# Optimization experiments

Hardware: AMD Instinct MI355X
Metric: run time of the kernel (lower is better)

Reference implementation:

```python
import jax, jax.numpy as jnp
import numpy as np

S = 64          # per-axis section size; sections = [64, 64, 64, 64], D = 256
N_TOK = 131072  # tokens
D = 256
FREQS = np.power(10000.0, -np.arange(18, dtype=np.float64) / 18.0).astype(np.float32)


def setup_inputs() -> dict:
    key = jax.random.key(0)
    k1, k2, k3 = jax.random.split(key, 3)
    return {
        "keyEmbeddings": jax.random.normal(k1, (N_TOK, D), dtype=jnp.float32),
        "queryEmbeddings": jax.random.normal(k2, (N_TOK, D), dtype=jnp.float32),
        "locations": jax.random.normal(k3, (N_TOK, 7), dtype=jnp.float32),
        "freqs": jnp.asarray(FREQS),
    }


def _rot(A, B, ang):
    # performRotation: newA = cos*A + sin*B ; newB = cos*B - sin*A
    c, s = jnp.cos(ang), jnp.sin(ang)
    return c * A + s * B, c * B - s * A


def reference(keyEmbeddings, queryEmbeddings, locations, freqs):
    K, Q, loc = keyEmbeddings, queryEmbeddings, locations
    a4, a5, a6 = loc[:, 4:5], loc[:, 5:6], loc[:, 6:7]

    # ---- stage 1: 3D axis-pair rotations ----
    qx, qy, qz, qr = Q[:, :S], Q[:, S:2*S], Q[:, 2*S:3*S], Q[:, 3*S:]
    qx, qy = _rot(qx, qy, -a4)
    qx, qz = _rot(qx, qz, -a5)
    qy, qz = _rot(qy, qz, -a6)
    Q = jnp.concatenate([qx, qy, qz, qr], axis=-1)

    kx, ky, kz, kr = K[:, :S], K[:, S:2*S], K[:, 2*S:3*S], K[:, 3*S:]
    ky, kz = _rot(ky, kz, a6)
    kx, kz = _rot(kx, kz, a5)
    kx, ky = _rot(kx, ky, a4)
    K = jnp.concatenate([kx, ky, kz, kr], axis=-1)

    # ---- stage 2: multi-frequency per-channel-pair rotations ----
    F = freqs.shape[0]
    P = 7 * F  # number of channel pairs (2*P <= D)
    ang = (loc[:, :, None] * freqs[None, None, :]).reshape(loc.shape[0], P)  # [N, P]
    c, s = jnp.cos(ang), jnp.sin(ang)

    # Faithful to the original in-place update: second element of each pair
    # uses the already-updated first element.
    Ka, Kb = K[:, 0:2*P:2], K[:, 1:2*P:2]
    Ka2 = c * Ka + s * Kb
    Kb2 = c * Kb - s * Ka2
    Kp = jnp.stack([Ka2, Kb2], axis=-1).reshape(K.shape[0], 2 * P)
    K = jnp.concatenate([Kp, K[:, 2*P:]], axis=-1)

    Qa, Qb = Q[:, 0:2*P:2], Q[:, 1:2*P:2]
    Qa2 = c * Qa - s * Qb
    Qb2 = c * Qb + s * Qa2
    Qp = jnp.stack([Qa2, Qb2], axis=-1).reshape(Q.shape[0], 2 * P)
    Q = jnp.concatenate([Qp, Q[:, 2*P:]], axis=-1)

    return K, Q
```

## Files before the change

### kernel.cpp

```cpp
#include <hip/hip_runtime.h>
#include <math.h>


namespace {

constexpr int kNTok = 131072;
constexpr int kD = 256;

__device__ __forceinline__ void pair_rot(int p, const float* lrow,
                                         const float* __restrict__ freqs,
                                         float& ka, float& kb,
                                         float& qa, float& qb) {
    const int j = p / 18;
    const int f = p - j * 18;
    const float ang = lrow[j] * freqs[f];
    float s, c;
    __sincosf(ang, &s, &c);
    float ka2 = fmaf(s, kb, c * ka);
    kb = fmaf(-s, ka2, c * kb);
    ka = ka2;
    float qa2 = fmaf(-s, qb, c * qa);
    qb = fmaf(s, qa2, c * qb);
    qa = qa2;
}

}

__global__ __launch_bounds__(256) void rope_kernel(
    const float* __restrict__ Kin, const float* __restrict__ Qin,
    const float* __restrict__ loc, const float* __restrict__ freqs,
    float* __restrict__ Kout, float* __restrict__ Qout)
{
    const int gtid = blockIdx.x * blockDim.x + threadIdx.x;
    const int n = gtid >> 4;
    const int u = gtid & 15;
    if (n >= kNTok) return;

    const size_t row = (size_t)n * kD;
    const float4* K4 = (const float4*)(Kin + row);
    const float4* Q4 = (const float4*)(Qin + row);
    float4 kx = K4[u], ky = K4[16 + u], kz = K4[32 + u], kr = K4[48 + u];
    float4 qx = Q4[u], qy = Q4[16 + u], qz = Q4[32 + u], qr = Q4[48 + u];

    const float* lrow = loc + (size_t)n * 7;
    float s4, c4, s5, c5, s6, c6;
    __sincosf(lrow[4], &s4, &c4);
    __sincosf(lrow[5], &s5, &c5);
    __sincosf(lrow[6], &s6, &c6);

#define ROT3(i)                                      \
    {                                                \
        float x = kx.i, y = ky.i, z = kz.i;          \
        float y1 = fmaf(s6, z, c6 * y);              \
        float z1 = fmaf(-s6, y, c6 * z);             \
        float x1 = fmaf(s5, z1, c5 * x);             \
        float z2 = fmaf(-s5, x, c5 * z1);            \
        kx.i = fmaf(s4, y1, c4 * x1);                \
        ky.i = fmaf(-s4, x1, c4 * y1);               \
        kz.i = z2;                                   \
        x = qx.i; y = qy.i; z = qz.i;                \
        float xq1 = fmaf(-s4, y, c4 * x);            \
        float yq1 = fmaf(s4, x, c4 * y);             \
        float xq2 = fmaf(-s5, z, c5 * xq1);          \
        float zq1 = fmaf(s5, xq1, c5 * z);           \
        qx.i = xq2;                                  \
        qy.i = fmaf(-s6, zq1, c6 * yq1);             \
        qz.i = fmaf(s6, yq1, c6 * zq1);              \
    }
    ROT3(x) ROT3(y) ROT3(z) ROT3(w)
#undef ROT3

    const int p0 = 2 * u;
    pair_rot(p0,          lrow, freqs, kx.x, kx.y, qx.x, qx.y);
    pair_rot(p0 + 1,      lrow, freqs, kx.z, kx.w, qx.z, qx.w);
    pair_rot(32 + p0,     lrow, freqs, ky.x, ky.y, qy.x, qy.y);
    pair_rot(32 + p0 + 1, lrow, freqs, ky.z, ky.w, qy.z, qy.w);
    pair_rot(64 + p0,     lrow, freqs, kz.x, kz.y, qz.x, qz.y);
    pair_rot(64 + p0 + 1, lrow, freqs, kz.z, kz.w, qz.z, qz.w);
    if (u < 15) {
        pair_rot(96 + p0,     lrow, freqs, kr.x, kr.y, qr.x, qr.y);
        pair_rot(96 + p0 + 1, lrow, freqs, kr.z, kr.w, qr.z, qr.w);
    }

    float4* Ko = (float4*)(Kout + row);
    float4* Qo = (float4*)(Qout + row);
    Ko[u] = kx; Ko[16 + u] = ky; Ko[32 + u] = kz; Ko[48 + u] = kr;
    Qo[u] = qx; Qo[16 + u] = qy; Qo[32 + u] = qz; Qo[48 + u] = qr;
}

extern "C" void kernel_launch(void* const* d_in, const int* in_sizes, int n_in,
                              void* d_out, int out_size, void* d_ws, size_t ws_size,
                              hipStream_t stream) {
    const float* K     = (const float*)d_in[0];
    const float* Q     = (const float*)d_in[1];
    const float* loc   = (const float*)d_in[2];
    const float* freqs = (const float*)d_in[3];
    float* Kout = (float*)d_out;
    float* Qout = Kout + (size_t)kNTok * kD;

    const int threads = 256;
    const int total_threads = kNTok * 16;
    const int blocks = (total_threads + threads - 1) / threads;
    hipLaunchKernelGGL(rope_kernel, dim3(blocks), dim3(threads), 0, stream,
                       K, Q, loc, freqs, Kout, Qout);
}
```

Measured before the change: 101.7 us.

## Split K and Q across separate threads and use nontemporal loads/stores

Launches twice as many threads, with the first half handling K rows and the second half Q rows, so each thread carries half the register state and there are more waves in flight. Global loads and stores of the embeddings become nontemporal vector accesses to avoid polluting the cache with streaming data. In exchange, the location row and its sines and cosines are loaded and computed twice, once per tensor.

```diff
diff --git a/kernel.cpp b/kernel.cpp
--- a/kernel.cpp
+++ b/kernel.cpp
@@ -6,22 +6,99 @@
 
 constexpr int kNTok = 131072;
 constexpr int kD = 256;
+constexpr int kHalfThreads = kNTok * 16;
 
-__device__ __forceinline__ void pair_rot(int p, const float* lrow,
+typedef float f4 __attribute__((ext_vector_type(4)));
+
+__device__ __forceinline__ f4 ntload(const float* p) {
+    return __builtin_nontemporal_load((const f4*)p);
+}
+__device__ __forceinline__ void ntstore(float* p, f4 v) {
+    __builtin_nontemporal_store(v, (f4*)p);
+}
+
+template <bool IS_K>
+__device__ __forceinline__ void pair_rot(int p, const float* __restrict__ lrow,
                                          const float* __restrict__ freqs,
-                                         float& ka, float& kb,
-                                         float& qa, float& qb) {
+                                         float& a, float& b) {
     const int j = p / 18;
     const int f = p - j * 18;
     const float ang = lrow[j] * freqs[f];
     float s, c;
     __sincosf(ang, &s, &c);
-    float ka2 = fmaf(s, kb, c * ka);
-    kb = fmaf(-s, ka2, c * kb);
-    ka = ka2;
-    float qa2 = fmaf(-s, qb, c * qa);
-    qb = fmaf(s, qa2, c * qb);
-    qa = qa2;
+    if constexpr (IS_K) {
+        float a2 = fmaf(s, b, c * a);
+        b = fmaf(-s, a2, c * b);
+        a = a2;
+    } else {
+        float a2 = fmaf(-s, b, c * a);
+        b = fmaf(s, a2, c * b);
+        a = a2;
+    }
+}
+
+template <bool IS_K>
+__device__ __forceinline__ void process(const float* __restrict__ in,
+                                        float* __restrict__ out,
+                                        const float* __restrict__ loc,
+                                        const float* __restrict__ freqs,
+                                        int n, int u) {
+    const size_t row = (size_t)n * kD;
+    const float* A = in + row;
+    f4 lx = ntload(A + 4 * u);
+    f4 ly = ntload(A + 64 + 4 * u);
+    f4 lz = ntload(A + 128 + 4 * u);
+    f4 lr = ntload(A + 192 + 4 * u);
+    float vx[4] = {lx.x, lx.y, lx.z, lx.w};
+    float vy[4] = {ly.x, ly.y, ly.z, ly.w};
+    float vz[4] = {lz.x, lz.y, lz.z, lz.w};
+    float vr[4] = {lr.x, lr.y, lr.z, lr.w};
+
+    const float* lrow = loc + (size_t)n * 7;
+    float s4, c4, s5, c5, s6, c6;
+    __sincosf(lrow[4], &s4, &c4);
+    __sincosf(lrow[5], &s5, &c5);
+    __sincosf(lrow[6], &s6, &c6);
+
+#pragma unroll
+    for (int i = 0; i < 4; ++i) {
+        float x = vx[i], y = vy[i], z = vz[i];
+        if constexpr (IS_K) {
+            float y1 = fmaf(s6, z, c6 * y);
+            float z1 = fmaf(-s6, y, c6 * z);
+            float x1 = fmaf(s5, z1, c5 * x);
+            float z2 = fmaf(-s5, x, c5 * z1);
+            vx[i] = fmaf(s4, y1, c4 * x1);
+            vy[i] = fmaf(-s4, x1, c4 * y1);
+            vz[i] = z2;
+        } else {
+            float x1 = fmaf(-s4, y, c4 * x);
+            float y1 = fmaf(s4, x, c4 * y);
+            float x2 = fmaf(-s5, z, c5 * x1);
+            float z1 = fmaf(s5, x1, c5 * z);
+            vx[i] = x2;
+            vy[i] = fmaf(-s6, z1, c6 * y1);
+            vz[i] = fmaf(s6, y1, c6 * z1);
+        }
+    }
+
+    const int p0 = 2 * u;
+    pair_rot<IS_K>(p0,          lrow, freqs, vx[0], vx[1]);
+    pair_rot<IS_K>(p0 + 1,      lrow, freqs, vx[2], vx[3]);
+    pair_rot<IS_K>(32 + p0,     lrow, freqs, vy[0], vy[1]);
+    pair_rot<IS_K>(32 + p0 + 1, lrow, freqs, vy[2], vy[3]);
+    pair_rot<IS_K>(64 + p0,     lrow, freqs, vz[0], vz[1]);
+    pair_rot<IS_K>(64 + p0 + 1, lrow, freqs, vz[2], vz[3]);
+    if (u < 15) {
+        pair_rot<IS_K>(96 + p0,     lrow, freqs, vr[0], vr[1]);
+        pair_rot<IS_K>(96 + p0 + 1, lrow, freqs, vr[2], vr[3]);
+    }
+
+    float* O = out + row;
+    ntstore(O + 4 * u,       f4{vx[0], vx[1], vx[2], vx[3]});
+    ntstore(O + 64 + 4 * u,  f4{vy[0], vy[1], vy[2], vy[3]});
+    ntstore(O + 128 + 4 * u, f4{vz[0], vz[1], vz[2], vz[3]});
+    ntstore(O + 192 + 4 * u, f4{vr[0], vr[1], vr[2], vr[3]});
 }
 
 }
@@ -32,60 +109,16 @@
     float* __restrict__ Kout, float* __restrict__ Qout)
 {
     const int gtid = blockIdx.x * blockDim.x + threadIdx.x;
-    const int n = gtid >> 4;
-    const int u = gtid & 15;
-    if (n >= kNTok) return;
-
-    const size_t row = (size_t)n * kD;
-    const float4* K4 = (const float4*)(Kin + row);
-    const float4* Q4 = (const float4*)(Qin + row);
-    float4 kx = K4[u], ky = K4[16 + u], kz = K4[32 + u], kr = K4[48 + u];
-    float4 qx = Q4[u], qy = Q4[16 + u], qz = Q4[32 + u], qr = Q4[48 + u];
-
-    const float* lrow = loc + (size_t)n * 7;
-    float s4, c4, s5, c5, s6, c6;
-    __sincosf(lrow[4], &s4, &c4);
-    __sincosf(lrow[5], &s5, &c5);
-    __sincosf(lrow[6], &s6, &c6);
-
-#define ROT3(i)                                      \
-    {                                                \
-        float x = kx.i, y = ky.i, z = kz.i;          \
-        float y1 = fmaf(s6, z, c6 * y);              \
-        float z1 = fmaf(-s6, y, c6 * z);             \
-        float x1 = fmaf(s5, z1, c5 * x);             \
-        float z2 = fmaf(-s5, x, c5 * z1);            \
-        kx.i = fmaf(s4, y1, c4 * x1);                \
-        ky.i = fmaf(-s4, x1, c4 * y1);               \
-        kz.i = z2;                                   \
-        x = qx.i; y = qy.i; z = qz.i;                \
-        float xq1 = fmaf(-s4, y, c4 * x);            \
-        float yq1 = fmaf(s4, x, c4 * y);             \
-        float xq2 = fmaf(-s5, z, c5 * xq1);          \
-        float zq1 = fmaf(s5, xq1, c5 * z);           \
-        qx.i = xq2;                                  \
-        qy.i = fmaf(-s6, zq1, c6 * yq1);             \
-        qz.i = fmaf(s6, yq1, c6 * zq1);              \
+    if (gtid < kHalfThreads) {
+        const int n = gtid >> 4;
+        const int u = gtid & 15;
+        process<true>(Kin, Kout, loc, freqs, n, u);
+    } else {
+        const int t = gtid - kHalfThreads;
+        const int n = t >> 4;
+        const int u = t & 15;
+        process<false>(Qin, Qout, loc, freqs, n, u);
     }
-    ROT3(x) ROT3(y) ROT3(z) ROT3(w)
-#undef ROT3
-
-    const int p0 = 2 * u;
-    pair_rot(p0,          lrow, freqs, kx.x, kx.y, qx.x, qx.y);
-    pair_rot(p0 + 1,      lrow, freqs, kx.z, kx.w, qx.z, qx.w);
-    pair_rot(32 + p0,     lrow, freqs, ky.x, ky.y, qy.x, qy.y);
-    pair_rot(32 + p0 + 1, lrow, freqs, ky.z, ky.w, qy.z, qy.w);
-    pair_rot(64 + p0,     lrow, freqs, kz.x, kz.y, qz.x, qz.y);
-    pair_rot(64 + p0 + 1, lrow, freqs, kz.z, kz.w, qz.z, qz.w);
-    if (u < 15) {
-        pair_rot(96 + p0,     lrow, freqs, kr.x, kr.y, qr.x, qr.y);
-        pair_rot(96 + p0 + 1, lrow, freqs, kr.z, kr.w, qr.z, qr.w);
-    }
-
-    float4* Ko = (float4*)(Kout + row);
-    float4* Qo = (float4*)(Qout + row);
-    Ko[u] = kx; Ko[16 + u] = ky; Ko[32 + u] = kz; Ko[48 + u] = kr;
-    Qo[u] = qx; Qo[16 + u] = qy; Qo[32 + u] = qz; Qo[48 + u] = qr;
 }
 
 extern "C" void kernel_launch(void* const* d_in, const int* in_sizes, int n_in,
@@ -99,8 +132,7 @@
     float* Qout = Kout + (size_t)kNTok * kD;
 
     const int threads = 256;
-    const int total_threads = kNTok * 16;
-    const int blocks = (total_threads + threads - 1) / threads;
+    const int blocks = (2 * kHalfThreads) / threads;
     hipLaunchKernelGGL(rope_kernel, dim3(blocks), dim3(threads), 0, stream,
                        K, Q, loc, freqs, Kout, Qout);
 }
```

Result: faster. 90.22 us (-11.3%).
